# Optimization experiments

Hardware: AMD Instinct MI355X
Metric: run time of the kernel (lower is better)

The kernel has to match this reference:

```python
import jax, jax.numpy as jnp
import numpy as np

PATCH = 16
EMB = 16
HID = 1024
B, S = 128, 4096
PAD_IDX = S  # max_sequence_length
PMAX = S // PATCH  # 256 patches max per sample
IN_DIM = PATCH + PATCH * EMB  # 272


def setup_inputs() -> dict:
    key = jax.random.key(0)
    ks = jax.random.split(key, 8)
    lengths = jax.random.randint(ks[0], (B,), 1, S + 1).astype(jnp.int32)
    vals = jax.random.normal(ks[1], (B, S), dtype=jnp.float32)
    # prefix-of-ones validity mask in the last feature channel
    mask = (jnp.arange(S)[None, :] < lengths[:, None]).astype(jnp.float32)
    x = jnp.stack([vals, mask], axis=-1)  # [B, S, 2]
    sc1 = 1.0 / np.sqrt(IN_DIM)
    sc2 = 1.0 / np.sqrt(HID)
    return {
        "x": x,
        "lengths": lengths,
        "pos_table": jax.random.normal(ks[2], (S + 1, EMB), dtype=jnp.float32),
        "W1": jax.random.uniform(ks[3], (IN_DIM, HID), jnp.float32, -sc1, sc1),
        "b1": jax.random.uniform(ks[4], (HID,), jnp.float32, -sc1, sc1),
        "W2": jax.random.uniform(ks[5], (HID, HID), jnp.float32, -sc2, sc2),
        "b2": jax.random.uniform(ks[6], (HID,), jnp.float32, -sc2, sc2),
    }


def reference(x, lengths, pos_table, W1, b1, W2, b2):
    # x: [B, S, 2] (value, mask); lengths[i] == mask[i].sum()
    t = jnp.arange(S)  # padded timeline, T = PMAX * PATCH == S
    vl = lengths[:, None]  # [B, 1]
    # pad each series to a multiple of PATCH by repeating its last valid value
    gather_idx = jnp.minimum(t[None, :], jnp.maximum(vl - 1, 0))  # [B, S]
    vals = jnp.take_along_axis(x[:, :, 0], gather_idx, axis=1)  # [B, S]
    pos = jnp.where(t[None, :] < vl, t[None, :], PAD_IDX)  # [B, S]
    vals_p = vals.reshape(B, PMAX, PATCH)
    pos_emb = pos_table[pos].reshape(B, PMAX, PATCH * EMB)  # gather + flatten
    feat = jnp.concatenate([vals_p, pos_emb], axis=-1)  # [B, PMAX, 272]
    h = jax.nn.gelu(feat @ W1 + b1, approximate=False)
    out = h @ W2 + b2  # [B, PMAX, HID]
    n_patch = (lengths + PATCH - 1) // PATCH  # [B]
    patch_mask = jnp.arange(PMAX)[None, :] < n_patch[:, None]
    out = out * patch_mask[:, :, None]  # zero rows beyond patch_cnt
    return out, n_patch
```

## Files before the change

### kernel.cpp

```cpp
#include <hip/hip_runtime.h>
#include <hip/hip_bf16.h>
#include <math.h>

#define NB     128
#define SLEN   4096
#define HID_   1024
#define INDIM_ 272
#define KPAD_  320
#define MFULL  32768
#define N_     1024

typedef __bf16 bf16x8 __attribute__((ext_vector_type(8)));
typedef float  f32x4  __attribute__((ext_vector_type(4)));
typedef __hip_bfloat16 hb;


__global__ void prep_w(const float* __restrict__ W1, const float* __restrict__ W2,
                       hb* __restrict__ w1t, hb* __restrict__ w2t) {
    __shared__ float tt[64][65];
    const int kt = blockIdx.x;
    const int nt = blockIdx.y;
    const int c = threadIdx.x & 63, r4 = threadIdx.x >> 6;
    if (kt < 5) {
#pragma unroll
        for (int j = 0; j < 16; ++j) {
            int r = j * 4 + r4;
            int k = kt * 64 + r;
            tt[r][c] = (k < INDIM_) ? W1[k * 1024 + nt * 64 + c] : 0.0f;
        }
        __syncthreads();
#pragma unroll
        for (int j = 0; j < 16; ++j) {
            int r = j * 4 + r4;
            w1t[(nt * 64 + r) * KPAD_ + kt * 64 + c] = __float2bfloat16(tt[c][r]);
        }
    } else {
        const int kw = kt - 5;
#pragma unroll
        for (int j = 0; j < 16; ++j) {
            int r = j * 4 + r4;
            tt[r][c] = W2[(kw * 64 + r) * 1024 + nt * 64 + c];
        }
        __syncthreads();
#pragma unroll
        for (int j = 0; j < 16; ++j) {
            int r = j * 4 + r4;
            w2t[(nt * 64 + r) * 1024 + kw * 64 + c] = __float2bfloat16(tt[c][r]);
        }
    }
}

__global__ __launch_bounds__(512) void build_feat_c(const float* __restrict__ x,
                                                    const int* __restrict__ lengths,
                                                    const float* __restrict__ pos_table,
                                                    hb* __restrict__ feat,
                                                    unsigned short* __restrict__ rowmap,
                                                    int* __restrict__ mc,
                                                    float* __restrict__ np_out) {
    __shared__ int scan[NB];
    const int b = blockIdx.x, t = threadIdx.x;
    const int chunk = blockIdx.y;
    if (t < NB) scan[t] = (lengths[t] + 15) >> 4;
    __syncthreads();
    for (int d = 1; d < NB; d <<= 1) {
        int v = 0;
        if (t < NB && t >= d) v = scan[t - d];
        __syncthreads();
        if (t < NB && t >= d) scan[t] += v;
        __syncthreads();
    }
    const int L = lengths[b];
    const int np = (L + 15) >> 4;
    const int off = scan[b] - np;
    if (b == 0 && chunk == 0) {
        if (t < NB) np_out[t] = (float)((lengths[t] + 15) >> 4);
        if (t == 0) *mc = scan[NB - 1];
    }
    const int p0 = chunk * 64;
    const int p1 = min(np, p0 + 64);
    if (p0 >= p1) return;
    const int cnt = p1 - p0;

    for (int p = p0 + t; p < p1; p += 512)
        rowmap[off + p] = (unsigned short)(b * 256 + p);

    const float* xb = x + (long)b * SLEN * 2;
    const int total = cnt * 40;
    for (int c = t; c < total; c += 512) {
        const int p = p0 + c / 40;
        const int j = c - (c / 40) * 40;
        const int col = j * 8;
        bf16x8 v;
        if (j < 2) {
#pragma unroll
            for (int e = 0; e < 8; ++e) {
                int tt2 = p * 16 + j * 8 + e;
                int idx = (tt2 < L) ? tt2 : (L - 1);
                v[e] = (__bf16)xb[(long)idx * 2];
            }
        } else if (col < INDIM_) {
            const int q = col - 16;
            const int tt2 = p * 16 + (q >> 4);
            const int pt = (tt2 < L) ? tt2 : SLEN;
            const float* src = pos_table + pt * 16 + (q & 15);
#pragma unroll
            for (int e = 0; e < 8; ++e) v[e] = (__bf16)src[e];
        } else {
            v = (bf16x8)0;
        }
        *(bf16x8*)(feat + (long)(off + p) * KPAD_ + col) = v;
    }
}


__device__ __forceinline__ void gl_lds16(const hb* g, hb* l) {
    __builtin_amdgcn_global_load_lds(
        (const __attribute__((address_space(1))) unsigned int*)g,
        (__attribute__((address_space(3))) unsigned int*)l, 16, 0, 0);
}

__device__ __forceinline__ float gelu_tanh(float v) {
    float u = 1.5957691216f * v * (1.0f + 0.044715f * v * v);
    float e = __expf(u);
    float th = (e - 1.0f) / (e + 1.0f);
    return 0.5f * v * (1.0f + th);
}

template <int MODE>
__global__ __launch_bounds__(512, 2) void gemm256(const hb* __restrict__ A,
                                                  const hb* __restrict__ BT,
                                                  const float* __restrict__ bias,
                                                  const unsigned short* __restrict__ rowmap,
                                                  const int* __restrict__ mc,
                                                  const int* __restrict__ lengths,
                                                  hb* __restrict__ HOut,
                                                  float* __restrict__ FOut,
                                                  int K, int nt) {
    __shared__ __align__(16) hb Sh[4][16384];

    const int tid = threadIdx.x;
    const int bid = blockIdx.x;

    if (MODE == 1 && bid >= 512) {
        const int zb = bid - 512;
        const int half = tid >> 8;
        const int c4 = tid & 255;
        for (int r = zb * 2 + half; r < MFULL; r += 1024) {
            const int b = r >> 8, p = r & 255;
            const int np = (lengths[b] + 15) >> 4;
            if (p >= np)
                *(f32x4*)(FOut + (long)r * N_ + c4 * 4) = (f32x4)0.0f;
        }
        return;
    }

    const int Mc = *mc;
    const int activeBm = (Mc + 255) >> 8;
    const int nActive = activeBm * 4;
    if (bid >= nActive) return;
    const int q = nActive >> 3, r = nActive & 7;
    const int xcd = bid & 7, idx = bid >> 3;
    const int wg = (xcd < r ? xcd * (q + 1) : r * (q + 1) + (xcd - r) * q) + idx;
    const int bm = wg >> 2;
    const int bn = wg & 3;

    const int wid = tid >> 6, lane = tid & 63;
    const int wr = wid >> 2, wc = wid & 3;
    const int fr = lane & 15, kg = lane >> 4;
    const int swz = (fr & 7) << 4;

    const long arow0 = (long)bm * 256;
    const int  brow0 = bn * 256;
    const hb* Bbase = BT + (long)brow0 * K;

    const int srow = tid >> 3;
    const int sel  = (((tid & 7) << 4) ^ ((srow & 7) << 4)) >> 1;
    const int ldst = tid * 8;

    f32x4 acc[8][4] = {};

    auto stage = [&](int t, int bsel) {
        const int k0 = t << 6;
#pragma unroll
        for (int j = 0; j < 4; ++j) {
            long gr = arow0 + j * 64 + srow;
            if (gr >= Mc) gr = Mc - 1;
            gl_lds16(A + gr * K + k0 + sel, &Sh[bsel][j * 4096 + ldst]);
        }
#pragma unroll
        for (int j = 0; j < 4; ++j)
            gl_lds16(Bbase + (long)(j * 64 + srow) * K + k0 + sel,
                     &Sh[2 + bsel][j * 4096 + ldst]);
    };

    stage(0, 0);
    stage(1, 1);
    asm volatile("s_waitcnt vmcnt(8)" ::: "memory");
    asm volatile("s_barrier" ::: "memory");

#define LDA_(dst, Ab, half)                                                  \
    _Pragma("unroll") for (int i = 0; i < 4; ++i)                            \
    _Pragma("unroll") for (int ks = 0; ks < 2; ++ks)                         \
        dst[i][ks] = *(const bf16x8*)((Ab) +                                 \
            (wr * 128 + (half) * 64 + i * 16 + fr) * 128 +                   \
            ((ks * 64 + kg * 16) ^ swz));

#define LDB_(Bb, half)                                                       \
    _Pragma("unroll") for (int jn = 0; jn < 2; ++jn)                         \
    _Pragma("unroll") for (int ks = 0; ks < 2; ++ks)                         \
        Bf[half][jn][ks] = *(const bf16x8*)((Bb) +                           \
            (wc * 64 + (half) * 32 + jn * 16 + fr) * 128 +                   \
            ((ks * 64 + kg * 16) ^ swz));

#define MFMA_QUAD(Aarr, a, b)                                                \
    __builtin_amdgcn_s_setprio(1);                                           \
    _Pragma("unroll") for (int ks = 0; ks < 2; ++ks)                         \
    _Pragma("unroll") for (int i = 0; i < 4; ++i)                            \
    _Pragma("unroll") for (int jn = 0; jn < 2; ++jn)                         \
        acc[(a) * 4 + i][(b) * 2 + jn] =                                     \
            __builtin_amdgcn_mfma_f32_16x16x32_bf16(                         \
                Aarr[i][ks], Bf[b][jn][ks], acc[(a) * 4 + i][(b) * 2 + jn],  \
                0, 0, 0);                                                    \
    __builtin_amdgcn_s_setprio(0);

    for (int t = 0; t < nt; ++t) {
        const char* Ab = (const char*)(&Sh[t & 1][0]);
        const char* Bb = (const char*)(&Sh[2 + (t & 1)][0]);
        bf16x8 A0[4][2], A1[4][2], Bf[2][2][2];

        LDB_(Bb, 0)
        LDA_(A0, Ab, 0)
        MFMA_QUAD(A0, 0, 0)
        LDB_(Bb, 1)
        MFMA_QUAD(A0, 0, 1)
        LDA_(A1, Ab, 1)
        MFMA_QUAD(A1, 1, 1)
        asm volatile("s_waitcnt lgkmcnt(0)" ::: "memory");
        asm volatile("s_barrier" ::: "memory");
        if (t + 2 < nt) stage(t + 2, t & 1);
        MFMA_QUAD(A1, 1, 0)
        if (t + 1 < nt) {
            if (t + 2 < nt) {
                asm volatile("s_waitcnt vmcnt(8)" ::: "memory");
            } else {
                asm volatile("s_waitcnt vmcnt(0)" ::: "memory");
            }
            asm volatile("s_barrier" ::: "memory");
        }
    }

    const int rbase = wr * 128 + kg * 4;
    const int cbase = wc * 64 + fr;
    float bvv[4];
#pragma unroll
    for (int ni = 0; ni < 4; ++ni) bvv[ni] = bias[bn * 256 + cbase + ni * 16];

    if (MODE == 0) {
        hb* Cs = (hb*)Sh;
#pragma unroll
        for (int ni = 0; ni < 4; ++ni) {
            const int col = cbase + ni * 16;
#pragma unroll
            for (int mi = 0; mi < 8; ++mi)
#pragma unroll
                for (int r2 = 0; r2 < 4; ++r2) {
                    float v = acc[mi][ni][r2] + bvv[ni];
                    Cs[(rbase + mi * 16 + r2) * 256 + col] = __float2bfloat16(gelu_tanh(v));
                }
        }
        __syncthreads();
        const hb* Cl = (const hb*)Sh;
#pragma unroll
        for (int c = 0; c < 16; ++c) {
            const int e = (c * 512 + tid) * 8;
            const int row = e >> 8, col = e & 255;
            bf16x8 v = *(const bf16x8*)(Cl + e);
            *(bf16x8*)(HOut + (arow0 + row) * N_ + bn * 256 + col) = v;
        }
    } else {
        float* Cf = (float*)Sh;
#pragma unroll
        for (int half = 0; half < 2; ++half) {
            if (half) __syncthreads();
            if ((wc >> 1) == half) {
#pragma unroll
                for (int ni = 0; ni < 4; ++ni) {
                    const int col = cbase + ni * 16 - half * 128;
#pragma unroll
                    for (int mi = 0; mi < 8; ++mi)
#pragma unroll
                        for (int r2 = 0; r2 < 4; ++r2)
                            Cf[(rbase + mi * 16 + r2) * 128 + col] =
                                acc[mi][ni][r2] + bvv[ni];
                }
            }
            __syncthreads();
#pragma unroll
            for (int c = 0; c < 16; ++c) {
                const int e = (c * 512 + tid) * 4;
                const int row = e >> 7, col = e & 127;
                const long cidx = arow0 + row;
                if (cidx < Mc) {
                    f32x4 v = *(const f32x4*)(Cf + e);
                    *(f32x4*)(FOut + (long)rowmap[cidx] * N_ + bn * 256 + half * 128 + col) = v;
                }
            }
        }
    }
}


extern "C" void kernel_launch(void* const* d_in, const int* in_sizes, int n_in,
                              void* d_out, int out_size, void* d_ws, size_t ws_size,
                              hipStream_t stream) {
    const float* x         = (const float*)d_in[0];
    const int*   lengths   = (const int*)d_in[1];
    const float* pos_table = (const float*)d_in[2];
    const float* W1        = (const float*)d_in[3];
    const float* b1        = (const float*)d_in[4];
    const float* W2        = (const float*)d_in[5];
    const float* b2        = (const float*)d_in[6];
    float* out = (float*)d_out;

    char* ws = (char*)d_ws;
    hb* w1t                = (hb*)(ws);
    hb* w2t                = (hb*)(ws + 655360);
    hb* feat               = (hb*)(ws + 2752512);
    hb* h                  = (hb*)(ws + 23724032);
    unsigned short* rowmap = (unsigned short*)(ws + 90832896);
    int* mc                = (int*)(ws + 90898432);

    hipLaunchKernelGGL(prep_w, dim3(21, 16), dim3(256), 0, stream, W1, W2, w1t, w2t);
    hipLaunchKernelGGL(build_feat_c, dim3(NB, 4), dim3(512), 0, stream,
                       x, lengths, pos_table, feat, rowmap, mc, out + (long)MFULL * N_);

    hipLaunchKernelGGL((gemm256<0>), dim3(512), dim3(512), 0, stream,
                       feat, w1t, b1, rowmap, mc, lengths, h, nullptr, KPAD_, KPAD_ / 64);
    hipLaunchKernelGGL((gemm256<1>), dim3(1024), dim3(512), 0, stream,
                       h, w2t, b2, rowmap, mc, lengths, nullptr, out, HID_, HID_ / 64);
}
```

Before: 102.6 us.

## Precompute positional-embedding projection per patch and replace first GEMM with rank-16 update

The first GEMM over the 272-wide feature vector is split algebraically. The positional-embedding part depends only on patch index, so it is precomputed once per patch (256x1024, bias included). Each row then only adds a 16-term value contribution in fp32 before GELU. Boundary patches that mix valid and padded positions are recomputed in a separate kernel using suffix sums of the pad embedding's projection. Output zeroing moves into the h-building kernel. This removes the feature-matrix build and the MFMA GEMM1 in exchange for fp32 CUDA-core work and an extra launch, and relies on the boundary kernel running after build_h to overwrite the last patch row.

```diff
diff --git a/kernel.cpp b/kernel.cpp
--- a/kernel.cpp
+++ b/kernel.cpp
@@ -5,119 +5,13 @@
 #define NB     128
 #define SLEN   4096
 #define HID_   1024
-#define INDIM_ 272
-#define KPAD_  320
 #define MFULL  32768
 #define N_     1024
 
 typedef __bf16 bf16x8 __attribute__((ext_vector_type(8)));
 typedef float  f32x4  __attribute__((ext_vector_type(4)));
+typedef float  f32x2  __attribute__((ext_vector_type(2)));
 typedef __hip_bfloat16 hb;
-
-
-__global__ void prep_w(const float* __restrict__ W1, const float* __restrict__ W2,
-                       hb* __restrict__ w1t, hb* __restrict__ w2t) {
-    __shared__ float tt[64][65];
-    const int kt = blockIdx.x;
-    const int nt = blockIdx.y;
-    const int c = threadIdx.x & 63, r4 = threadIdx.x >> 6;
-    if (kt < 5) {
-#pragma unroll
-        for (int j = 0; j < 16; ++j) {
-            int r = j * 4 + r4;
-            int k = kt * 64 + r;
-            tt[r][c] = (k < INDIM_) ? W1[k * 1024 + nt * 64 + c] : 0.0f;
-        }
-        __syncthreads();
-#pragma unroll
-        for (int j = 0; j < 16; ++j) {
-            int r = j * 4 + r4;
-            w1t[(nt * 64 + r) * KPAD_ + kt * 64 + c] = __float2bfloat16(tt[c][r]);
-        }
-    } else {
-        const int kw = kt - 5;
-#pragma unroll
-        for (int j = 0; j < 16; ++j) {
-            int r = j * 4 + r4;
-            tt[r][c] = W2[(kw * 64 + r) * 1024 + nt * 64 + c];
-        }
-        __syncthreads();
-#pragma unroll
-        for (int j = 0; j < 16; ++j) {
-            int r = j * 4 + r4;
-            w2t[(nt * 64 + r) * 1024 + kw * 64 + c] = __float2bfloat16(tt[c][r]);
-        }
-    }
-}
-
-__global__ __launch_bounds__(512) void build_feat_c(const float* __restrict__ x,
-                                                    const int* __restrict__ lengths,
-                                                    const float* __restrict__ pos_table,
-                                                    hb* __restrict__ feat,
-                                                    unsigned short* __restrict__ rowmap,
-                                                    int* __restrict__ mc,
-                                                    float* __restrict__ np_out) {
-    __shared__ int scan[NB];
-    const int b = blockIdx.x, t = threadIdx.x;
-    const int chunk = blockIdx.y;
-    if (t < NB) scan[t] = (lengths[t] + 15) >> 4;
-    __syncthreads();
-    for (int d = 1; d < NB; d <<= 1) {
-        int v = 0;
-        if (t < NB && t >= d) v = scan[t - d];
-        __syncthreads();
-        if (t < NB && t >= d) scan[t] += v;
-        __syncthreads();
-    }
-    const int L = lengths[b];
-    const int np = (L + 15) >> 4;
-    const int off = scan[b] - np;
-    if (b == 0 && chunk == 0) {
-        if (t < NB) np_out[t] = (float)((lengths[t] + 15) >> 4);
-        if (t == 0) *mc = scan[NB - 1];
-    }
-    const int p0 = chunk * 64;
-    const int p1 = min(np, p0 + 64);
-    if (p0 >= p1) return;
-    const int cnt = p1 - p0;
-
-    for (int p = p0 + t; p < p1; p += 512)
-        rowmap[off + p] = (unsigned short)(b * 256 + p);
-
-    const float* xb = x + (long)b * SLEN * 2;
-    const int total = cnt * 40;
-    for (int c = t; c < total; c += 512) {
-        const int p = p0 + c / 40;
-        const int j = c - (c / 40) * 40;
-        const int col = j * 8;
-        bf16x8 v;
-        if (j < 2) {
-#pragma unroll
-            for (int e = 0; e < 8; ++e) {
-                int tt2 = p * 16 + j * 8 + e;
-                int idx = (tt2 < L) ? tt2 : (L - 1);
-                v[e] = (__bf16)xb[(long)idx * 2];
-            }
-        } else if (col < INDIM_) {
-            const int q = col - 16;
-            const int tt2 = p * 16 + (q >> 4);
-            const int pt = (tt2 < L) ? tt2 : SLEN;
-            const float* src = pos_table + pt * 16 + (q & 15);
-#pragma unroll
-            for (int e = 0; e < 8; ++e) v[e] = (__bf16)src[e];
-        } else {
-            v = (bf16x8)0;
-        }
-        *(bf16x8*)(feat + (long)(off + p) * KPAD_ + col) = v;
-    }
-}
-
-
-__device__ __forceinline__ void gl_lds16(const hb* g, hb* l) {
-    __builtin_amdgcn_global_load_lds(
-        (const __attribute__((address_space(1))) unsigned int*)g,
-        (__attribute__((address_space(3))) unsigned int*)l, 16, 0, 0);
-}
 
 __device__ __forceinline__ float gelu_tanh(float v) {
     float u = 1.5957691216f * v * (1.0f + 0.044715f * v * v);
@@ -126,37 +20,229 @@
     return 0.5f * v * (1.0f + th);
 }
 
-template <int MODE>
-__global__ __launch_bounds__(512, 2) void gemm256(const hb* __restrict__ A,
-                                                  const hb* __restrict__ BT,
-                                                  const float* __restrict__ bias,
-                                                  const unsigned short* __restrict__ rowmap,
-                                                  const int* __restrict__ mc,
+__global__ __launch_bounds__(256) void prep_all(const float* __restrict__ W1,
+                                                const float* __restrict__ b1,
+                                                const float* __restrict__ W2,
+                                                const float* __restrict__ pos_table,
+                                                const int* __restrict__ lengths,
+                                                hb* __restrict__ w2t,
+                                                float* __restrict__ Pb,
+                                                float* __restrict__ SUF,
+                                                unsigned short* __restrict__ rowmap,
+                                                int* __restrict__ meta,
+                                                float* __restrict__ np_out) {
+    const int bid = blockIdx.x;
+    const int t = threadIdx.x;
+
+    if (bid < 256) {
+        __shared__ float tt[64][65];
+        const int kt = bid >> 4, nt = bid & 15;
+        const int c = t & 63, r4 = t >> 6;
+#pragma unroll
+        for (int j = 0; j < 16; ++j) {
+            int r = j * 4 + r4;
+            tt[r][c] = W2[(kt * 64 + r) * 1024 + nt * 64 + c];
+        }
+        __syncthreads();
+#pragma unroll
+        for (int j = 0; j < 16; ++j) {
+            int r = j * 4 + r4;
+            w2t[(nt * 64 + r) * 1024 + kt * 64 + c] = __float2bfloat16(tt[c][r]);
+        }
+    } else if (bid < 512) {
+        __shared__ float pl[8 * 256];
+        const int id = bid - 256;
+        const int pg = id >> 3;
+        const int cgb = (id & 7) * 128;
+#pragma unroll
+        for (int i = 0; i < 8; ++i) {
+            int idx = t + i * 256;
+            pl[idx] = pos_table[pg * 8 * 256 + idx];
+        }
+        __syncthreads();
+        const int prow = t >> 5;
+        const int c0 = cgb + (t & 31) * 4;
+        f32x4 acc = *(const f32x4*)&b1[c0];
+        const float* pr = &pl[prow * 256];
+#pragma unroll 4
+        for (int k = 0; k < 256; ++k)
+            acc += pr[k] * *(const f32x4*)&W1[(16 + k) * 1024 + c0];
+        *(f32x4*)&Pb[(pg * 8 + prow) * 1024 + c0] = acc;
+    } else if (bid < 516) {
+        const int c = (bid - 512) * 256 + t;
+        float padv[16];
+#pragma unroll
+        for (int e = 0; e < 16; ++e) padv[e] = pos_table[4096 * 16 + e];
+        float tmp[16];
+#pragma unroll
+        for (int j = 0; j < 16; ++j) {
+            float s = 0.0f;
+#pragma unroll
+            for (int e = 0; e < 16; ++e)
+                s += padv[e] * W1[(16 + 16 * j + e) * 1024 + c];
+            tmp[j] = s;
+        }
+        float run = 0.0f;
+        SUF[16 * 1024 + c] = 0.0f;
+        for (int m = 15; m >= 0; --m) {
+            run += tmp[m];
+            SUF[m * 1024 + c] = run;
+        }
+    } else {
+        __shared__ int sc[NB], sNp[NB];
+        if (t < NB) { sNp[t] = (lengths[t] + 15) >> 4; sc[t] = sNp[t]; }
+        __syncthreads();
+        for (int d = 1; d < NB; d <<= 1) {
+            int v = 0;
+            if (t < NB && t >= d) v = sc[t - d];
+            __syncthreads();
+            if (t < NB && t >= d) sc[t] += v;
+            __syncthreads();
+        }
+        if (t < NB) {
+            meta[t] = sc[t] - sNp[t];
+            np_out[t] = (float)sNp[t];
+        }
+        if (t == 0) meta[NB] = sc[NB - 1];
+        __syncthreads();
+        for (int b = 0; b < NB; ++b) {
+            const int off = sc[b] - sNp[b], np = sNp[b];
+            for (int p = t; p < np; p += 256)
+                rowmap[off + p] = (unsigned short)(b * 256 + p);
+        }
+    }
+}
+
+__global__ __launch_bounds__(512) void build_h(const float* __restrict__ x,
+                                               const int* __restrict__ lengths,
+                                               const float* __restrict__ W1,
+                                               const float* __restrict__ Pb,
+                                               const unsigned short* __restrict__ rowmap,
+                                               const int* __restrict__ meta,
+                                               hb* __restrict__ h,
+                                               float* __restrict__ out) {
+    const int bid = blockIdx.x;
+    const int t = threadIdx.x;
+
+    for (int r = bid; r < MFULL; r += 2048) {
+        const int b = r >> 8, p = r & 255;
+        const int np = (lengths[b] + 15) >> 4;
+        if (p >= np)
+            *(f32x2*)(out + (long)r * N_ + t * 2) = (f32x2)0.0f;
+    }
+
+    const int Mc = meta[NB];
+    const int gr0 = bid * 16;
+    if (gr0 >= Mc) return;
+
+    __shared__ float vals[16][16];
+    __shared__ int rinfo[16];
+    if (t < 16) rinfo[t] = (gr0 + t < Mc) ? (int)rowmap[gr0 + t] : -1;
+    __syncthreads();
+    if (t < 256) {
+        const int row = t >> 4, j = t & 15;
+        const int ri = rinfo[row];
+        if (ri >= 0) {
+            const int b = ri >> 8, p = ri & 255;
+            const int L = lengths[b];
+            const int tt = p * 16 + j;
+            const int idx = (tt < L) ? tt : (L - 1);
+            vals[row][j] = x[((long)b * SLEN + idx) * 2];
+        }
+    }
+    __syncthreads();
+
+    const int row = t >> 5, cg = t & 31;
+    const int ri = rinfo[row];
+    if (ri < 0) return;
+    const int p = ri & 255;
+
+    f32x4 a[4][2];
+#pragma unroll
+    for (int i = 0; i < 4; ++i) {
+        const int c0 = i * 256 + cg * 8;
+        a[i][0] = *(const f32x4*)&Pb[p * 1024 + c0];
+        a[i][1] = *(const f32x4*)&Pb[p * 1024 + c0 + 4];
+    }
+#pragma unroll
+    for (int j = 0; j < 16; ++j) {
+        const float s = vals[row][j];
+        const float* wj = &W1[j * 1024];
+#pragma unroll
+        for (int i = 0; i < 4; ++i) {
+            const int c0 = i * 256 + cg * 8;
+            a[i][0] += s * *(const f32x4*)&wj[c0];
+            a[i][1] += s * *(const f32x4*)&wj[c0 + 4];
+        }
+    }
+    hb* hr = h + (long)(gr0 + row) * 1024;
+#pragma unroll
+    for (int i = 0; i < 4; ++i) {
+        bf16x8 o;
+#pragma unroll
+        for (int e = 0; e < 4; ++e) o[e] = (__bf16)gelu_tanh(a[i][0][e]);
+#pragma unroll
+        for (int e = 0; e < 4; ++e) o[4 + e] = (__bf16)gelu_tanh(a[i][1][e]);
+        *(bf16x8*)(hr + i * 256 + cg * 8) = o;
+    }
+}
+
+__global__ __launch_bounds__(256) void boundary_h(const float* __restrict__ x,
                                                   const int* __restrict__ lengths,
-                                                  hb* __restrict__ HOut,
-                                                  float* __restrict__ FOut,
-                                                  int K, int nt) {
+                                                  const float* __restrict__ W1,
+                                                  const float* __restrict__ b1,
+                                                  const float* __restrict__ pos_table,
+                                                  const float* __restrict__ SUF,
+                                                  const int* __restrict__ meta,
+                                                  hb* __restrict__ h) {
+    const int b = blockIdx.x;
+    const int t = threadIdx.x;
+    const int L = lengths[b];
+    const int np = (L + 15) >> 4;
+    const int p = np - 1;
+    const int m = L - p * 16;
+    const long gr = meta[b] + p;
+    const int c0 = t * 4;
+
+    f32x4 acc = *(const f32x4*)&SUF[m * 1024 + c0];
+    acc += *(const f32x4*)&b1[c0];
+#pragma unroll
+    for (int j = 0; j < 16; ++j) {
+        const int tt = p * 16 + j;
+        const int idx = (tt < L) ? tt : (L - 1);
+        const float v = x[((long)b * SLEN + idx) * 2];
+        acc += v * *(const f32x4*)&W1[j * 1024 + c0];
+    }
+    const int km = m * 16;
+    const float* pf = pos_table + p * 256;
+    for (int k = 0; k < km; ++k)
+        acc += pf[k] * *(const f32x4*)&W1[(16 + k) * 1024 + c0];
+
+    hb* hr = h + gr * 1024 + c0;
+#pragma unroll
+    for (int e = 0; e < 4; ++e) hr[e] = __float2bfloat16(gelu_tanh(acc[e]));
+}
+
+
+__device__ __forceinline__ void gl_lds16(const hb* g, hb* l) {
+    __builtin_amdgcn_global_load_lds(
+        (const __attribute__((address_space(1))) unsigned int*)g,
+        (__attribute__((address_space(3))) unsigned int*)l, 16, 0, 0);
+}
+
+__global__ __launch_bounds__(512, 2) void gemm_out(const hb* __restrict__ A,
+                                                   const hb* __restrict__ BT,
+                                                   const float* __restrict__ bias,
+                                                   const unsigned short* __restrict__ rowmap,
+                                                   const int* __restrict__ meta,
+                                                   float* __restrict__ FOut) {
     __shared__ __align__(16) hb Sh[4][16384];
-
-    const int tid = threadIdx.x;
-    const int bid = blockIdx.x;
-
-    if (MODE == 1 && bid >= 512) {
-        const int zb = bid - 512;
-        const int half = tid >> 8;
-        const int c4 = tid & 255;
-        for (int r = zb * 2 + half; r < MFULL; r += 1024) {
-            const int b = r >> 8, p = r & 255;
-            const int np = (lengths[b] + 15) >> 4;
-            if (p >= np)
-                *(f32x4*)(FOut + (long)r * N_ + c4 * 4) = (f32x4)0.0f;
-        }
-        return;
-    }
-
-    const int Mc = *mc;
+    const int K = 1024, nt = 16;
+
+    const int Mc = meta[NB];
     const int activeBm = (Mc + 255) >> 8;
     const int nActive = activeBm * 4;
+    const int bid = blockIdx.x;
     if (bid >= nActive) return;
     const int q = nActive >> 3, r = nActive & 7;
     const int xcd = bid & 7, idx = bid >> 3;
@@ -164,6 +250,7 @@
     const int bm = wg >> 2;
     const int bn = wg & 3;
 
+    const int tid = threadIdx.x;
     const int wid = tid >> 6, lane = tid & 63;
     const int wr = wid >> 2, wc = wid & 3;
     const int fr = lane & 15, kg = lane >> 4;
@@ -255,55 +342,31 @@
 #pragma unroll
     for (int ni = 0; ni < 4; ++ni) bvv[ni] = bias[bn * 256 + cbase + ni * 16];
 
-    if (MODE == 0) {
-        hb* Cs = (hb*)Sh;
-#pragma unroll
-        for (int ni = 0; ni < 4; ++ni) {
-            const int col = cbase + ni * 16;
-#pragma unroll
-            for (int mi = 0; mi < 8; ++mi)
-#pragma unroll
-                for (int r2 = 0; r2 < 4; ++r2) {
-                    float v = acc[mi][ni][r2] + bvv[ni];
-                    Cs[(rbase + mi * 16 + r2) * 256 + col] = __float2bfloat16(gelu_tanh(v));
-                }
+    float* Cf = (float*)Sh;
+#pragma unroll
+    for (int half = 0; half < 2; ++half) {
+        if (half) __syncthreads();
+        if ((wc >> 1) == half) {
+#pragma unroll
+            for (int ni = 0; ni < 4; ++ni) {
+                const int col = cbase + ni * 16 - half * 128;
+#pragma unroll
+                for (int mi = 0; mi < 8; ++mi)
+#pragma unroll
+                    for (int r2 = 0; r2 < 4; ++r2)
+                        Cf[(rbase + mi * 16 + r2) * 128 + col] =
+                            acc[mi][ni][r2] + bvv[ni];
+            }
         }
         __syncthreads();
-        const hb* Cl = (const hb*)Sh;
 #pragma unroll
         for (int c = 0; c < 16; ++c) {
-            const int e = (c * 512 + tid) * 8;
-            const int row = e >> 8, col = e & 255;
-            bf16x8 v = *(const bf16x8*)(Cl + e);
-            *(bf16x8*)(HOut + (arow0 + row) * N_ + bn * 256 + col) = v;
-        }
-    } else {
-        float* Cf = (float*)Sh;
-#pragma unroll
-        for (int half = 0; half < 2; ++half) {
-            if (half) __syncthreads();
-            if ((wc >> 1) == half) {
-#pragma unroll
-                for (int ni = 0; ni < 4; ++ni) {
-                    const int col = cbase + ni * 16 - half * 128;
-#pragma unroll
-                    for (int mi = 0; mi < 8; ++mi)
-#pragma unroll
-                        for (int r2 = 0; r2 < 4; ++r2)
-                            Cf[(rbase + mi * 16 + r2) * 128 + col] =
-                                acc[mi][ni][r2] + bvv[ni];
-                }
-            }
-            __syncthreads();
-#pragma unroll
-            for (int c = 0; c < 16; ++c) {
-                const int e = (c * 512 + tid) * 4;
-                const int row = e >> 7, col = e & 127;
-                const long cidx = arow0 + row;
-                if (cidx < Mc) {
-                    f32x4 v = *(const f32x4*)(Cf + e);
-                    *(f32x4*)(FOut + (long)rowmap[cidx] * N_ + bn * 256 + half * 128 + col) = v;
-                }
+            const int e = (c * 512 + tid) * 4;
+            const int row = e >> 7, col = e & 127;
+            const long cidx = arow0 + row;
+            if (cidx < Mc) {
+                f32x4 v = *(const f32x4*)(Cf + e);
+                *(f32x4*)(FOut + (long)rowmap[cidx] * N_ + bn * 256 + half * 128 + col) = v;
             }
         }
     }
@@ -323,19 +386,20 @@
     float* out = (float*)d_out;
 
     char* ws = (char*)d_ws;
-    hb* w1t                = (hb*)(ws);
-    hb* w2t                = (hb*)(ws + 655360);
-    hb* feat               = (hb*)(ws + 2752512);
-    hb* h                  = (hb*)(ws + 23724032);
-    unsigned short* rowmap = (unsigned short*)(ws + 90832896);
-    int* mc                = (int*)(ws + 90898432);
-
-    hipLaunchKernelGGL(prep_w, dim3(21, 16), dim3(256), 0, stream, W1, W2, w1t, w2t);
-    hipLaunchKernelGGL(build_feat_c, dim3(NB, 4), dim3(512), 0, stream,
-                       x, lengths, pos_table, feat, rowmap, mc, out + (long)MFULL * N_);
-
-    hipLaunchKernelGGL((gemm256<0>), dim3(512), dim3(512), 0, stream,
-                       feat, w1t, b1, rowmap, mc, lengths, h, nullptr, KPAD_, KPAD_ / 64);
-    hipLaunchKernelGGL((gemm256<1>), dim3(1024), dim3(512), 0, stream,
-                       h, w2t, b2, rowmap, mc, lengths, nullptr, out, HID_, HID_ / 64);
-}
+    hb* w2t                = (hb*)(ws);
+    hb* h                  = (hb*)(ws + 2097152);
+    float* Pb              = (float*)(ws + 69206016);
+    float* SUF             = (float*)(ws + 70254592);
+    unsigned short* rowmap = (unsigned short*)(ws + 70324224);
+    int* meta              = (int*)(ws + 70389760);
+
+    hipLaunchKernelGGL(prep_all, dim3(517), dim3(256), 0, stream,
+                       W1, b1, W2, pos_table, lengths, w2t, Pb, SUF, rowmap, meta,
+                       out + (long)MFULL * N_);
+    hipLaunchKernelGGL(build_h, dim3(2048), dim3(512), 0, stream,
+                       x, lengths, W1, Pb, rowmap, meta, h, out);
+    hipLaunchKernelGGL(boundary_h, dim3(NB), dim3(256), 0, stream,
+                       x, lengths, W1, b1, pos_table, SUF, meta, h);
+    hipLaunchKernelGGL(gemm_out, dim3(512), dim3(512), 0, stream,
+                       h, w2t, b2, rowmap, meta, out);
+}
```

Result: slower. 219.8 us (+114.2%).
